# Kernel optimization log

Hardware: AMD Instinct MI355X
Metric: run time of the kernel (lower is better)

## Reference

```python
import jax, jax.numpy as jnp
import numpy as np

N_USER = 100000
N_ITEM = 100000
E = 1000000
D_IN = 64
D_OUT = 64


def setup_inputs() -> dict:
    key = jax.random.key(0)
    ks = jax.random.split(key, 10)
    scale = 1.0 / np.sqrt(D_IN)
    return {
        "feat_user": jax.random.normal(ks[0], (N_USER, D_IN), jnp.float32),
        "feat_item": jax.random.normal(ks[1], (N_ITEM, D_IN), jnp.float32),
        "src_clicks": jax.random.randint(ks[2], (E,), 0, N_USER),        # user ids
        "dst_clicks": jax.random.randint(ks[3], (E,), 0, N_ITEM),        # item ids
        "src_clicked_by": jax.random.randint(ks[4], (E,), 0, N_ITEM),    # item ids
        "dst_clicked_by": jax.random.randint(ks[5], (E,), 0, N_USER),    # user ids
        "W_clicks": jax.random.normal(ks[6], (D_OUT, D_IN), jnp.float32) * scale,
        "b_clicks": jax.random.normal(ks[7], (D_OUT,), jnp.float32) * scale,
        "W_clicked_by": jax.random.normal(ks[8], (D_OUT, D_IN), jnp.float32) * scale,
        "b_clicked_by": jax.random.normal(ks[9], (D_OUT,), jnp.float32) * scale,
    }


def _relation_mean(feat_src, W, b, src, dst, n_dst):
    # per-relation Linear on src features (nn.Linear: x @ W.T + b)
    Wh = feat_src @ W.T + b                                  # [N_src, D_OUT]
    # copy_u + mean: gather messages along edges, segment-mean at dst
    msum = jax.ops.segment_sum(Wh[src], dst, num_segments=n_dst)   # [n_dst, D_OUT]
    deg = jax.ops.segment_sum(jnp.ones(src.shape[0], jnp.float32), dst,
                              num_segments=n_dst)                   # [n_dst]
    return msum / jnp.maximum(deg, 1.0)[:, None]             # zero-degree dsts -> 0


def reference(feat_user, feat_item, src_clicks, dst_clicks,
              src_clicked_by, dst_clicked_by,
              W_clicks, b_clicks, W_clicked_by, b_clicked_by):
    # relation (user, clicks, item): messages land on item nodes
    h_item = _relation_mean(feat_user, W_clicks, b_clicks,
                            src_clicks, dst_clicks, N_ITEM)
    # relation (item, clicked_by, user): messages land on user nodes
    h_user = _relation_mean(feat_item, W_clicked_by, b_clicked_by,
                            src_clicked_by, dst_clicked_by, N_USER)
    # cross-relation 'sum' reducer: each ntype receives from exactly one relation here
    return (h_user, h_item)
```

## Files before the change

### kernel.cpp

```cpp
#include <hip/hip_runtime.h>

#define D 64
#define BSH 7
#define BK 128
#define NBK 1024
#define CAP 2048
#define CHUNK 4096
#define EPT (CHUNK / 256)
#define TILE 64

static __device__ __forceinline__ unsigned short f2bf(float x) {
    unsigned int u = __float_as_uint(x);
    unsigned int r = (u + 0x7FFFu + ((u >> 16) & 1u)) >> 16;
    return (unsigned short)r;
}

__global__ __launch_bounds__(256) void phase1(
    const float* __restrict__ feat_u, const float* __restrict__ feat_i,
    const float* __restrict__ W_c, const float* __restrict__ b_c,
    const float* __restrict__ W_cb, const float* __restrict__ b_cb,
    unsigned short* __restrict__ Whb_u, unsigned short* __restrict__ Whb_i,
    const int* __restrict__ srcA, const int* __restrict__ dstA,
    const int* __restrict__ srcB, const int* __restrict__ dstB,
    int* __restrict__ bcur,
    unsigned int* __restrict__ ebufA, unsigned int* __restrict__ ebufB,
    int n_user, int n_item, int n_edges, int ntile, int eb) {
    __shared__ union {
        struct { float FT[D * TILE]; float WT[D * TILE]; } lin;
        struct { int hist[NBK], cur[NBK]; } fil;
    } sh;
    int t = threadIdx.x;
    int blk = blockIdx.x;

    if (blk < 2 * ntile) {
        int rel = (blk >= ntile);
        int tile = rel ? blk - ntile : blk;
        const float* feat = rel ? feat_i : feat_u;
        const float* W    = rel ? W_cb   : W_c;
        const float* bia  = rel ? b_cb   : b_c;
        unsigned short* out = rel ? Whb_i : Whb_u;
        int n = rel ? n_item : n_user;
        int row0 = tile * TILE;
        if (row0 >= n) return;
        int lr = t >> 4;
        int kq = t & 15;
        int k4 = kq * 4;
        #pragma unroll
        for (int it = 0; it < 4; ++it) {
            int r = lr + it * 16;
            int grow = row0 + r; if (grow > n - 1) grow = n - 1;
            float4 f = *(const float4*)(feat + (size_t)grow * D + k4);
            int sw = (((r >> 2) ^ kq) & 15) * 4 + (r & 3);
            sh.lin.FT[(k4 + 0) * TILE + sw] = f.x;
            sh.lin.FT[(k4 + 1) * TILE + sw] = f.y;
            sh.lin.FT[(k4 + 2) * TILE + sw] = f.z;
            sh.lin.FT[(k4 + 3) * TILE + sw] = f.w;
            float4 w = *(const float4*)(W + r * D + k4);
            sh.lin.WT[(k4 + 0) * TILE + sw] = w.x;
            sh.lin.WT[(k4 + 1) * TILE + sw] = w.y;
            sh.lin.WT[(k4 + 2) * TILE + sw] = w.z;
            sh.lin.WT[(k4 + 3) * TILE + sw] = w.w;
        }
        __syncthreads();
        int cbW = t & 15;
        int cbF = t >> 4;
        int c0 = cbW * 4;
        int r0 = cbF * 4;
        float4 bv = *(const float4*)(bia + c0);
        float acc[4][4];
        #pragma unroll
        for (int ri = 0; ri < 4; ++ri) {
            acc[ri][0] = bv.x; acc[ri][1] = bv.y; acc[ri][2] = bv.z; acc[ri][3] = bv.w;
        }
        #pragma unroll 8
        for (int k = 0; k < D; ++k) {
            int kq2 = k >> 2;
            float4 w = *(const float4*)(sh.lin.WT + k * TILE + (((cbW ^ kq2) & 15) << 2));
            float4 f = *(const float4*)(sh.lin.FT + k * TILE + (((cbF ^ kq2) & 15) << 2));
            acc[0][0] = fmaf(f.x, w.x, acc[0][0]); acc[0][1] = fmaf(f.x, w.y, acc[0][1]);
            acc[0][2] = fmaf(f.x, w.z, acc[0][2]); acc[0][3] = fmaf(f.x, w.w, acc[0][3]);
            acc[1][0] = fmaf(f.y, w.x, acc[1][0]); acc[1][1] = fmaf(f.y, w.y, acc[1][1]);
            acc[1][2] = fmaf(f.y, w.z, acc[1][2]); acc[1][3] = fmaf(f.y, w.w, acc[1][3]);
            acc[2][0] = fmaf(f.z, w.x, acc[2][0]); acc[2][1] = fmaf(f.z, w.y, acc[2][1]);
            acc[2][2] = fmaf(f.z, w.z, acc[2][2]); acc[2][3] = fmaf(f.z, w.w, acc[2][3]);
            acc[3][0] = fmaf(f.w, w.x, acc[3][0]); acc[3][1] = fmaf(f.w, w.y, acc[3][1]);
            acc[3][2] = fmaf(f.w, w.z, acc[3][2]); acc[3][3] = fmaf(f.w, w.w, acc[3][3]);
        }
        #pragma unroll
        for (int ri = 0; ri < 4; ++ri) {
            int row = row0 + r0 + ri;
            if (row < n) {
                ushort4 o;
                o.x = f2bf(acc[ri][0]); o.y = f2bf(acc[ri][1]);
                o.z = f2bf(acc[ri][2]); o.w = f2bf(acc[ri][3]);
                *(ushort4*)(out + (size_t)row * D + c0) = o;
            }
        }
    } else {
        int fb = blk - 2 * ntile;
        int rel = (fb >= eb);
        int chunk = rel ? fb - eb : fb;
        const int* src = rel ? srcB : srcA;
        const int* dst = rel ? dstB : dstA;
        int* bu = bcur + rel * NBK;
        unsigned int* ebuf = rel ? ebufB : ebufA;
        int base = chunk * CHUNK;
        int m = n_edges - base; if (m > CHUNK) m = CHUNK;
        unsigned int packed[EPT];
        int bk[EPT];
        if (m == CHUNK) {
            const int4* s4p = (const int4*)(src + base);
            const int4* d4p = (const int4*)(dst + base);
            int4 sv[EPT / 4], dv[EPT / 4];
            #pragma unroll
            for (int q = 0; q < EPT / 4; ++q) {
                sv[q] = s4p[t * (EPT / 4) + q];
                dv[q] = d4p[t * (EPT / 4) + q];
            }
            for (int i = t; i < NBK; i += 256) sh.fil.hist[i] = 0;
            __syncthreads();
            #pragma unroll
            for (int q = 0; q < EPT / 4; ++q) {
                int s4a[4] = {sv[q].x, sv[q].y, sv[q].z, sv[q].w};
                int d4a[4] = {dv[q].x, dv[q].y, dv[q].z, dv[q].w};
                #pragma unroll
                for (int jj = 0; jj < 4; ++jj) {
                    int j = q * 4 + jj;
                    bk[j] = ((unsigned)d4a[jj]) >> BSH;
                    packed[j] = (unsigned int)s4a[jj] | (((unsigned int)d4a[jj] & (BK - 1)) << 24);
                    atomicAdd(&sh.fil.hist[bk[j]], 1);
                }
            }
        } else {
            for (int i = t; i < NBK; i += 256) sh.fil.hist[i] = 0;
            __syncthreads();
            #pragma unroll
            for (int j = 0; j < EPT; ++j) {
                int e = base + t * EPT + j;
                if (e < n_edges) {
                    int d = dst[e];
                    int s = src[e];
                    bk[j] = ((unsigned)d) >> BSH;
                    packed[j] = (unsigned int)s | (((unsigned int)d & (BK - 1)) << 24);
                    atomicAdd(&sh.fil.hist[bk[j]], 1);
                } else bk[j] = -1;
            }
        }
        __syncthreads();
        for (int b2 = t; b2 < NBK; b2 += 256) {
            int c = sh.fil.hist[b2];
            if (c) sh.fil.cur[b2] = b2 * CAP + atomicAdd(&bu[b2], c);
        }
        __syncthreads();
        #pragma unroll
        for (int j = 0; j < EPT; ++j) {
            if (bk[j] >= 0) {
                int pos = atomicAdd(&sh.fil.cur[bk[j]], 1);
                if ((unsigned)(pos - bk[j] * CAP) < CAP)
                    ebuf[pos] = packed[j];
            }
        }
    }
}

__global__ __launch_bounds__(256) void bucket_gather(
    const unsigned short* __restrict__ Whb_u, const unsigned short* __restrict__ Whb_i,
    const unsigned int* __restrict__ ebufA, const unsigned int* __restrict__ ebufB,
    const int* __restrict__ bcur,
    float* __restrict__ h_user, float* __restrict__ h_item,
    int n_user, int n_item) {
    int rel = blockIdx.y;
    const unsigned short* Wh = rel ? Whb_u : Whb_i;
    const unsigned int* ebuf = rel ? ebufB : ebufA;
    float* out = rel ? h_item : h_user;
    int n = rel ? n_item : n_user;
    int b = blockIdx.x;
    int cnt = bcur[rel * NBK + b]; if (cnt > CAP) cnt = CAP;
    size_t base = (size_t)b * CAP;
    __shared__ unsigned int ssrc[CAP];
    __shared__ int hist[BK], ofs[BK], cur[BK];
    __shared__ int w0tot;
    int t = threadIdx.x;
    if (t < BK) hist[t] = 0;
    __syncthreads();
    unsigned int pk[CAP / 256];
    #pragma unroll
    for (int j = 0; j < CAP / 256; ++j) {
        int i = t + j * 256;
        if (i < cnt) {
            pk[j] = ebuf[base + i];
            atomicAdd(&hist[pk[j] >> 24], 1);
        }
    }
    __syncthreads();
    {
        int lane = t & 63;
        int v = (t < BK) ? hist[t] : 0;
        int inc = v;
        #pragma unroll
        for (int o = 1; o < 64; o <<= 1) {
            int x = __shfl_up(inc, o, 64);
            if (lane >= o) inc += x;
        }
        if (t == 63) w0tot = inc;
        __syncthreads();
        if (t >= 64 && t < BK) inc += w0tot;
        if (t < BK) { int ex = inc - v; ofs[t] = ex; cur[t] = ex; }
    }
    __syncthreads();
    #pragma unroll
    for (int j = 0; j < CAP / 256; ++j) {
        int i = t + j * 256;
        if (i < cnt) {
            int nd = pk[j] >> 24;
            int p = atomicAdd(&cur[nd], 1);
            ssrc[p] = pk[j] & 0xFFFFFFu;
        }
    }
    __syncthreads();
    int lane = t & 63;
    int w = t >> 6;
    int half = lane >> 5;
    int lp = lane & 31;
    int node0 = b * BK;
    for (int nd = w; nd < BK; nd += 4) {
        int node = node0 + nd;
        if (node >= n) break;
        int st = ofs[nd];
        int dg = hist[nd];
        int en = st + dg;
        float l[8], h[8];
        #pragma unroll
        for (int q = 0; q < 8; ++q) { l[q] = 0.f; h[q] = 0.f; }
        for (int j = st; j < en; j += 16) {
            unsigned int v[8];
            #pragma unroll
            for (int q = 0; q < 8; ++q) {
                int e = j + 2 * q + half;
                v[q] = 0;
                if (e < en) v[q] = ((const unsigned int*)(Wh + (size_t)ssrc[e] * D))[lp];
            }
            #pragma unroll
            for (int q = 0; q < 8; ++q) {
                l[q] += __uint_as_float(v[q] << 16);
                h[q] += __uint_as_float(v[q] & 0xFFFF0000u);
            }
        }
        float lo = ((l[0] + l[1]) + (l[2] + l[3])) + ((l[4] + l[5]) + (l[6] + l[7]));
        float hi = ((h[0] + h[1]) + (h[2] + h[3])) + ((h[4] + h[5]) + (h[6] + h[7]));
        lo += __shfl_xor(lo, 32, 64);
        hi += __shfl_xor(hi, 32, 64);
        if (half == 0) {
            float inv = 1.f / fmaxf((float)dg, 1.f);
            float2 o; o.x = lo * inv; o.y = hi * inv;
            *(float2*)(out + (size_t)node * D + 2 * lp) = o;
        }
    }
}

extern "C" void kernel_launch(void* const* d_in, const int* in_sizes, int n_in,
                              void* d_out, int out_size, void* d_ws, size_t ws_size,
                              hipStream_t stream) {
    const float* feat_user      = (const float*)d_in[0];
    const float* feat_item      = (const float*)d_in[1];
    const int*   src_clicks     = (const int*)d_in[2];
    const int*   dst_clicks     = (const int*)d_in[3];
    const int*   src_clicked_by = (const int*)d_in[4];
    const int*   dst_clicked_by = (const int*)d_in[5];
    const float* W_clicks       = (const float*)d_in[6];
    const float* b_clicks       = (const float*)d_in[7];
    const float* W_clicked_by   = (const float*)d_in[8];
    const float* b_clicked_by   = (const float*)d_in[9];

    const int n_user  = in_sizes[0] / D;
    const int n_item  = in_sizes[1] / D;
    const int n_edges = in_sizes[2];

    float* out = (float*)d_out;
    float* h_user = out;
    float* h_item = out + (size_t)n_user * D;

    unsigned short* Whb_user = (unsigned short*)d_ws;
    unsigned short* Whb_item = Whb_user + (size_t)n_user * D;
    int* ip        = (int*)(Whb_item + (size_t)n_item * D);
    unsigned int* ebuf_user = (unsigned int*)ip;  ip += NBK * CAP;
    unsigned int* ebuf_item = (unsigned int*)ip;  ip += NBK * CAP;
    int* bcur = ip;

    hipMemsetAsync(bcur, 0, 2 * NBK * sizeof(int), stream);

    int ntile = (max(n_user, n_item) + TILE - 1) / TILE;
    int eb = (n_edges + CHUNK - 1) / CHUNK;
    phase1<<<2 * ntile + 2 * eb, 256, 0, stream>>>(
        feat_user, feat_item, W_clicks, b_clicks, W_clicked_by, b_clicked_by,
        Whb_user, Whb_item,
        src_clicked_by, dst_clicked_by, src_clicks, dst_clicks,
        bcur, ebuf_user, ebuf_item,
        n_user, n_item, n_edges, ntile, eb);

    int nbkt = (max(n_user, n_item) + BK - 1) / BK;
    bucket_gather<<<dim3(nbkt, 2), 256, 0, stream>>>(
        Whb_user, Whb_item, ebuf_user, ebuf_item, bcur,
        h_user, h_item, n_user, n_item);
}
```

Before: 218.8 us.

## Double linear-transform row tile to 128 with 8x4 register blocking per thread

The dense Linear stage in phase1 now processes 128 source rows per block instead of 64. Each thread computes an 8x4 output block, so every W value read from shared memory feeds twice as many FMAs. W is stored separately as a 64x64 swizzled tile, and the feature swizzle is widened to 32 groups. This halves the number of linear-transform blocks and the per-row W staging, at the cost of more registers per thread and more shared memory, which may reduce occupancy. ntile must be computed from TILE on the host for the change to be consistent.

Result: faster. 208.2 us (-4.8%).

```diff
diff --git a/kernel.cpp b/kernel.cpp
--- a/kernel.cpp
+++ b/kernel.cpp
@@ -7,7 +7,7 @@
 #define CAP 2048
 #define CHUNK 4096
 #define EPT (CHUNK / 256)
-#define TILE 64
+#define TILE 128
 
 static __device__ __forceinline__ unsigned short f2bf(float x) {
     unsigned int u = __float_as_uint(x);
@@ -26,7 +26,7 @@
     unsigned int* __restrict__ ebufA, unsigned int* __restrict__ ebufB,
     int n_user, int n_item, int n_edges, int ntile, int eb) {
     __shared__ union {
-        struct { float FT[D * TILE]; float WT[D * TILE]; } lin;
+        struct { float FT[D * TILE]; float WT[D * D]; } lin;
         struct { int hist[NBK], cur[NBK]; } fil;
     } sh;
     int t = threadIdx.x;
@@ -42,52 +42,58 @@
         int n = rel ? n_item : n_user;
         int row0 = tile * TILE;
         if (row0 >= n) return;
-        int lr = t >> 4;
         int kq = t & 15;
+        int rr = t >> 4;
         int k4 = kq * 4;
         #pragma unroll
-        for (int it = 0; it < 4; ++it) {
-            int r = lr + it * 16;
+        for (int g = 0; g < 8; ++g) {
+            int r = rr + g * 16;
             int grow = row0 + r; if (grow > n - 1) grow = n - 1;
             float4 f = *(const float4*)(feat + (size_t)grow * D + k4);
-            int sw = (((r >> 2) ^ kq) & 15) * 4 + (r & 3);
+            int sw = ((((r >> 2) ^ kq) & 31) << 2) + (r & 3);
             sh.lin.FT[(k4 + 0) * TILE + sw] = f.x;
             sh.lin.FT[(k4 + 1) * TILE + sw] = f.y;
             sh.lin.FT[(k4 + 2) * TILE + sw] = f.z;
             sh.lin.FT[(k4 + 3) * TILE + sw] = f.w;
-            float4 w = *(const float4*)(W + r * D + k4);
-            sh.lin.WT[(k4 + 0) * TILE + sw] = w.x;
-            sh.lin.WT[(k4 + 1) * TILE + sw] = w.y;
-            sh.lin.WT[(k4 + 2) * TILE + sw] = w.z;
-            sh.lin.WT[(k4 + 3) * TILE + sw] = w.w;
+        }
+        #pragma unroll
+        for (int g = 0; g < 4; ++g) {
+            int c = rr + g * 16;
+            float4 w = *(const float4*)(W + c * D + k4);
+            int swc = ((((c >> 2) ^ kq) & 15) << 2) + (c & 3);
+            sh.lin.WT[(k4 + 0) * D + swc] = w.x;
+            sh.lin.WT[(k4 + 1) * D + swc] = w.y;
+            sh.lin.WT[(k4 + 2) * D + swc] = w.z;
+            sh.lin.WT[(k4 + 3) * D + swc] = w.w;
         }
         __syncthreads();
-        int cbW = t & 15;
-        int cbF = t >> 4;
-        int c0 = cbW * 4;
-        int r0 = cbF * 4;
+        int cb = t & 15;
+        int rb = t >> 4;
+        int c0 = cb * 4;
+        int r0 = rb * 8;
         float4 bv = *(const float4*)(bia + c0);
-        float acc[4][4];
-        #pragma unroll
-        for (int ri = 0; ri < 4; ++ri) {
+        float acc[8][4];
+        #pragma unroll
+        for (int ri = 0; ri < 8; ++ri) {
             acc[ri][0] = bv.x; acc[ri][1] = bv.y; acc[ri][2] = bv.z; acc[ri][3] = bv.w;
         }
-        #pragma unroll 8
+        #pragma unroll 4
         for (int k = 0; k < D; ++k) {
             int kq2 = k >> 2;
-            float4 w = *(const float4*)(sh.lin.WT + k * TILE + (((cbW ^ kq2) & 15) << 2));
-            float4 f = *(const float4*)(sh.lin.FT + k * TILE + (((cbF ^ kq2) & 15) << 2));
-            acc[0][0] = fmaf(f.x, w.x, acc[0][0]); acc[0][1] = fmaf(f.x, w.y, acc[0][1]);
-            acc[0][2] = fmaf(f.x, w.z, acc[0][2]); acc[0][3] = fmaf(f.x, w.w, acc[0][3]);
-            acc[1][0] = fmaf(f.y, w.x, acc[1][0]); acc[1][1] = fmaf(f.y, w.y, acc[1][1]);
-            acc[1][2] = fmaf(f.y, w.z, acc[1][2]); acc[1][3] = fmaf(f.y, w.w, acc[1][3]);
-            acc[2][0] = fmaf(f.z, w.x, acc[2][0]); acc[2][1] = fmaf(f.z, w.y, acc[2][1]);
-            acc[2][2] = fmaf(f.z, w.z, acc[2][2]); acc[2][3] = fmaf(f.z, w.w, acc[2][3]);
-            acc[3][0] = fmaf(f.w, w.x, acc[3][0]); acc[3][1] = fmaf(f.w, w.y, acc[3][1]);
-            acc[3][2] = fmaf(f.w, w.z, acc[3][2]); acc[3][3] = fmaf(f.w, w.w, acc[3][3]);
-        }
-        #pragma unroll
-        for (int ri = 0; ri < 4; ++ri) {
+            float4 w  = *(const float4*)(sh.lin.WT + k * D    + (((cb ^ kq2) & 15) << 2));
+            float4 fA = *(const float4*)(sh.lin.FT + k * TILE + ((((rb * 2)     ^ kq2) & 31) << 2));
+            float4 fB = *(const float4*)(sh.lin.FT + k * TILE + ((((rb * 2 + 1) ^ kq2) & 31) << 2));
+            float fr[8] = {fA.x, fA.y, fA.z, fA.w, fB.x, fB.y, fB.z, fB.w};
+            #pragma unroll
+            for (int ri = 0; ri < 8; ++ri) {
+                acc[ri][0] = fmaf(fr[ri], w.x, acc[ri][0]);
+                acc[ri][1] = fmaf(fr[ri], w.y, acc[ri][1]);
+                acc[ri][2] = fmaf(fr[ri], w.z, acc[ri][2]);
+                acc[ri][3] = fmaf(fr[ri], w.w, acc[ri][3]);
+            }
+        }
+        #pragma unroll
+        for (int ri = 0; ri < 8; ++ri) {
             int row = row0 + r0 + ri;
             if (row < n) {
                 ushort4 o;
```
